# Kernel optimization log

Hardware: AMD Instinct MI355X
Metric: run time of the kernel (lower is better)

The kernel has to match this reference:

```python
import jax, jax.numpy as jnp
import numpy as np

N_NODES = 100000
N_EDGES = 1600000
IN_CH = 61
OUT_CH = 64
BN_EPS = 1e-5


def setup_inputs() -> dict:
    key = jax.random.key(0)
    ks = jax.random.split(key, 8)
    x = jax.random.normal(ks[0], (N_NODES, IN_CH), dtype=jnp.float32)
    pos = jax.random.normal(ks[1], (N_NODES, 3), dtype=jnp.float32)
    edge_index = jax.random.randint(ks[2], (2, N_EDGES), 0, N_NODES, dtype=jnp.int64)
    d_in = 3 + IN_CH  # 64
    W1 = jax.random.normal(ks[3], (d_in, OUT_CH), dtype=jnp.float32) / np.sqrt(d_in)
    b1 = jnp.zeros((OUT_CH,), dtype=jnp.float32)
    g1 = jnp.ones((OUT_CH,), dtype=jnp.float32)
    be1 = jnp.zeros((OUT_CH,), dtype=jnp.float32)
    Wg = jax.random.normal(ks[4], (OUT_CH, 1), dtype=jnp.float32) / np.sqrt(OUT_CH)
    bg = jnp.zeros((1,), dtype=jnp.float32)
    gg = jnp.ones((1,), dtype=jnp.float32)
    bgb = jnp.zeros((1,), dtype=jnp.float32)
    return {"x": x, "pos": pos, "edge_index": edge_index,
            "W1": W1, "b1": b1, "g1": g1, "be1": be1,
            "Wg": Wg, "bg": bg, "gg": gg, "bgb": bgb}


def _bn_act(h, gamma, beta):
    # PyG MLP layer: BatchNorm1d (training-mode batch stats) -> SiLU
    mu = h.mean(axis=0)
    var = h.var(axis=0)
    h = (h - mu) * jax.lax.rsqrt(var + BN_EPS) * gamma + beta
    return jax.nn.silu(h)


def reference(x, pos, edge_index, W1, b1, g1, be1, Wg, bg, gg, bgb):
    src = edge_index[0]  # source node j (messages flow j -> i)
    dst = edge_index[1]  # target node i
    n = x.shape[0]
    # PointNetConv message: local_nn(cat([x_j, pos_j - pos_i]))
    feat = jnp.concatenate([x[src], pos[src] - pos[dst]], axis=-1)  # [E, 3+in]
    h = _bn_act(feat @ W1 + b1, g1, be1)  # [E, out]
    # AttentionalAggregation gate: MLP([out, 1]) per edge
    gate = _bn_act(h @ Wg + bg, gg, bgb)  # [E, 1]
    # segment softmax over destination nodes
    m = jax.ops.segment_max(gate, dst, num_segments=n)  # [N, 1]
    e = jnp.exp(gate - m[dst])
    s = jax.ops.segment_sum(e, dst, num_segments=n)
    alpha = e / (s[dst] + 1e-16)
    # weighted scatter-sum aggregate
    out = jax.ops.segment_sum(alpha * h, dst, num_segments=n)  # [N, out]
    return out
```

## Files before the change

kernel.cpp:

```cpp
#include <hip/hip_runtime.h>
#include <hip/hip_bf16.h>
#include <math.h>

constexpr int N_NODES = 100000;
constexpr int N_EDGES = 1600000;
constexpr int IN_CH   = 61;
constexpr float BN_EPS = 1e-5f;
constexpr int NPART   = 32;

constexpr int S_PH = 192;
constexpr int S_PG = 192 + NPART * 128;
constexpr int S_TOT = S_PG + NPART * 2;

typedef float f32x4 __attribute__((ext_vector_type(4)));
typedef short s16x8 __attribute__((ext_vector_type(8)));

__device__ __forceinline__ float silu(float x) { return x / (1.0f + expf(-x)); }

__device__ __forceinline__ float bf2f(unsigned v) { return __uint_as_float(v << 16); }
__device__ __forceinline__ unsigned f2bf(float f) {
    unsigned u = __float_as_uint(f);
    return (u + 0x7FFFu + ((u >> 16) & 1u)) >> 16;
}

__device__ __forceinline__ bool edge_gemm(
    int e, const float* __restrict__ x, const float* __restrict__ pos,
    const int* __restrict__ ei, const float* __restrict__ W1,
    const float* __restrict__ b1, float* acc, int* jd_out)
{
    int js = ei[e];
    int jd = ei[N_EDGES + e];
    *jd_out = jd;
    bool valid = ((unsigned)js < (unsigned)N_NODES) && ((unsigned)jd < (unsigned)N_NODES);
    if (!valid) {
        #pragma unroll
        for (int c = 0; c < 64; ++c) acc[c] = 0.0f;
        return false;
    }
    #pragma unroll
    for (int c = 0; c < 64; ++c) acc[c] = b1[c];
    const float* xr = x + (size_t)js * IN_CH;
    #pragma unroll 4
    for (int k = 0; k < IN_CH; ++k) {
        float fk = xr[k];
        #pragma unroll
        for (int c = 0; c < 64; ++c) acc[c] += fk * W1[k * 64 + c];
    }
    #pragma unroll
    for (int j = 0; j < 3; ++j) {
        float fk = pos[js * 3 + j] - pos[jd * 3 + j];
        #pragma unroll
        for (int c = 0; c < 64; ++c) acc[c] += fk * W1[(IN_CH + j) * 64 + c];
    }
    return true;
}

__global__ __launch_bounds__(256) void k_init(float* stats, int* deg) {
    int i = blockIdx.x * 256 + threadIdx.x;
    if (i < S_TOT) stats[i] = 0.0f;
    if (i < N_NODES) deg[i] = 0;
}

__global__ __launch_bounds__(256) void k_prep(const float* __restrict__ W1,
                                              short* __restrict__ wf)
{
    int i = blockIdx.x * 256 + threadIdx.x;
    int j    = i & 7;
    int lane = (i >> 3) & 63;
    int kc   = (i >> 9) & 1;
    int ct   = i >> 10;
    int c = ct * 16 + (lane & 15);
    int k = kc * 32 + (lane >> 4) * 8 + j;
    float v = W1[k * 64 + c];
    unsigned hi = f2bf(v);
    unsigned lo = f2bf(v - bf2f(hi));
    wf[i] = (short)hi;
    wf[4096 + i] = (short)lo;
}

__global__ __launch_bounds__(256) void k_edge_mfma(
    const float* __restrict__ x, const float* __restrict__ pos,
    const int* __restrict__ ei, const short* __restrict__ wf,
    const float* __restrict__ b1, float* __restrict__ stats,
    int* __restrict__ deg, void* __restrict__ h, size_t h_cap)
{
    __shared__ __align__(16) short fsh[64][72];
    __shared__ __align__(16) short fsl[64][72];
    __shared__ float lsum[128];

    const int tid  = threadIdx.x;
    const int w    = tid >> 6, lane = tid & 63;
    const int e0   = blockIdx.x * 64;

    if (tid < 128) lsum[tid] = 0.0f;

    int js_l = 0, jd_l = 0;
    if (lane < 16) {
        int e = e0 + w * 16 + lane;
        js_l = ei[e];
        jd_l = ei[N_EDGES + e];
        if ((unsigned)js_l >= (unsigned)N_NODES) js_l = 0;
        if ((unsigned)jd_l >= (unsigned)N_NODES) jd_l = 0;
        atomicAdd(&deg[jd_l], 1);
    }

    #pragma unroll 4
    for (int j = 0; j < 16; ++j) {
        int js = __shfl(js_l, j);
        int jd = __shfl(jd_l, j);
        int r  = w * 16 + j;
        float v;
        if (lane < IN_CH) v = x[(size_t)js * IN_CH + lane];
        else              v = pos[js * 3 + (lane - IN_CH)] - pos[jd * 3 + (lane - IN_CH)];
        unsigned hi = f2bf(v);
        unsigned lo = f2bf(v - bf2f(hi));
        fsh[r][lane] = (short)hi;
        fsl[r][lane] = (short)lo;
    }
    __syncthreads();

    const int r = lane & 15, g = lane >> 4;
    const int arow = w * 16 + r;
    s16x8 ah0 = *(const s16x8*)&fsh[arow][g * 8];
    s16x8 ah1 = *(const s16x8*)&fsh[arow][32 + g * 8];
    s16x8 al0 = *(const s16x8*)&fsl[arow][g * 8];
    s16x8 al1 = *(const s16x8*)&fsl[arow][32 + g * 8];

    const bool do_h = ((size_t)(e0 + 64) * 128 <= h_cap);
    unsigned short* hp = (unsigned short*)h;

    #pragma unroll
    for (int ct = 0; ct < 4; ++ct) {
        int c = ct * 16 + r;
        s16x8 bh0 = *(const s16x8*)&wf[((ct * 2 + 0) * 64 + lane) * 8];
        s16x8 bh1 = *(const s16x8*)&wf[((ct * 2 + 1) * 64 + lane) * 8];
        s16x8 bl0 = *(const s16x8*)&wf[4096 + ((ct * 2 + 0) * 64 + lane) * 8];
        s16x8 bl1 = *(const s16x8*)&wf[4096 + ((ct * 2 + 1) * 64 + lane) * 8];
        f32x4 acc = {0.0f, 0.0f, 0.0f, 0.0f};
        acc = __builtin_amdgcn_mfma_f32_16x16x32_bf16(al0, bh0, acc, 0, 0, 0);
        acc = __builtin_amdgcn_mfma_f32_16x16x32_bf16(al1, bh1, acc, 0, 0, 0);
        acc = __builtin_amdgcn_mfma_f32_16x16x32_bf16(ah0, bl0, acc, 0, 0, 0);
        acc = __builtin_amdgcn_mfma_f32_16x16x32_bf16(ah1, bl1, acc, 0, 0, 0);
        acc = __builtin_amdgcn_mfma_f32_16x16x32_bf16(ah0, bh0, acc, 0, 0, 0);
        acc = __builtin_amdgcn_mfma_f32_16x16x32_bf16(ah1, bh1, acc, 0, 0, 0);
        float bias = b1[c];
        float s = 0.0f, q = 0.0f;
        #pragma unroll
        for (int i = 0; i < 4; ++i) {
            unsigned hb = f2bf(acc[i] + bias);
            float v = bf2f(hb);
            s += v; q += v * v;
            if (do_h) {
                int row = w * 16 + g * 4 + i;
                hp[(size_t)(e0 + row) * 64 + c] = (unsigned short)hb;
            }
        }
        s += __shfl_xor(s, 16); s += __shfl_xor(s, 32);
        q += __shfl_xor(q, 16); q += __shfl_xor(q, 32);
        if (g == 0) {
            atomicAdd(&lsum[c], s);
            atomicAdd(&lsum[64 + c], q);
        }
    }
    __syncthreads();
    if (tid < 128)
        atomicAdd(&stats[S_PH + (blockIdx.x & (NPART - 1)) * 128 + tid], lsum[tid]);
}

template<int MODE>
__global__ __launch_bounds__(128) void k_edge(
    const float* __restrict__ x, const float* __restrict__ pos,
    const int* __restrict__ ei, const float* __restrict__ W1,
    const float* __restrict__ b1, float* __restrict__ stats,
    int* __restrict__ deg, void* __restrict__ h, size_t h_cap)
{
    constexpr int EPB = 128;
    __shared__ float fs[EPB][65];
    __shared__ float ls[128];

    const int tid  = threadIdx.x;
    const int wave = tid >> 6, lane = tid & 63;
    const int eb   = blockIdx.x * EPB;
    const int r0   = wave * 64;

    const int eg = eb + r0 + lane;
    int js_l = ei[eg];
    int jd_l = ei[N_EDGES + eg];
    bool valid = ((unsigned)js_l < (unsigned)N_NODES) &&
                 ((unsigned)jd_l < (unsigned)N_NODES);
    if (valid) atomicAdd(&deg[jd_l], 1);

    if constexpr (MODE == 2) {
        if (tid < 128) ls[tid] = 0.0f;
    }

    for (int j = 0; j < 64; ++j) {
        int js = __shfl(js_l, j);
        int jd = __shfl(jd_l, j);
        int ok = __shfl((int)valid, j);
        int r = r0 + j;
        if (lane < IN_CH) {
            fs[r][lane] = ok ? x[(size_t)js * IN_CH + lane] : 0.0f;
        } else {
            int d = lane - IN_CH;
            fs[r][lane] = ok ? (pos[js * 3 + d] - pos[jd * 3 + d]) : 0.0f;
        }
    }
    __syncthreads();

    #pragma unroll 1
    for (int half = 0; half < 2; ++half) {
        const int base = half * 32;
        float acc[32];
        #pragma unroll
        for (int c = 0; c < 32; ++c) acc[c] = valid ? b1[base + c] : 0.0f;
        if (valid) {
            #pragma unroll 4
            for (int k = 0; k < 64; ++k) {
                float fk = fs[tid][k];
                #pragma unroll
                for (int c = 0; c < 32; ++c)
                    acc[c] += fk * W1[k * 64 + base + c];
            }
        }
        if constexpr (MODE == 0) {
            if ((size_t)(eb + tid + 1) * 256 <= h_cap) {
                float4* hq = (float4*)((char*)h + (size_t)(eb + tid) * 256
                                       + (size_t)base * 4);
                #pragma unroll
                for (int i = 0; i < 8; ++i)
                    hq[i] = make_float4(acc[4*i], acc[4*i+1], acc[4*i+2], acc[4*i+3]);
            }
        } else {
            #pragma unroll
            for (int c = 0; c < 32; ++c) {
                atomicAdd(&ls[base + c], acc[c]);
                atomicAdd(&ls[64 + base + c], acc[c] * acc[c]);
            }
        }
    }

    if constexpr (MODE == 2) {
        __syncthreads();
        if (tid < 128)
            atomicAdd(&stats[S_PH + (blockIdx.x & (NPART-1)) * 128 + tid], ls[tid]);
    }
}

template<int MODE>
__global__ __launch_bounds__(256) void k_stats(const void* __restrict__ h,
                                               float* __restrict__ stats)
{
    constexpr int VEC = (MODE == 0) ? 4 : 8;
    const size_t nvec = (size_t)N_EDGES * 64 / VEC;
    size_t stride = (size_t)gridDim.x * 256;
    size_t g0 = (size_t)blockIdx.x * 256 + threadIdx.x;
    int c0 = (int)((g0 * VEC) & 63);
    float sum[VEC], sq[VEC];
    #pragma unroll
    for (int j = 0; j < VEC; ++j) { sum[j] = 0.0f; sq[j] = 0.0f; }

    for (size_t v = g0; v < nvec; v += stride) {
        float vals[VEC];
        if constexpr (MODE == 0) {
            float4 t = ((const float4*)h)[v];
            vals[0] = t.x; vals[1] = t.y; vals[2] = t.z; vals[3] = t.w;
        } else {
            uint4 t = ((const uint4*)h)[v];
            vals[0] = bf2f(t.x & 0xFFFF); vals[1] = bf2f(t.x >> 16);
            vals[2] = bf2f(t.y & 0xFFFF); vals[3] = bf2f(t.y >> 16);
            vals[4] = bf2f(t.z & 0xFFFF); vals[5] = bf2f(t.z >> 16);
            vals[6] = bf2f(t.w & 0xFFFF); vals[7] = bf2f(t.w >> 16);
        }
        #pragma unroll
        for (int j = 0; j < VEC; ++j) { sum[j] += vals[j]; sq[j] += vals[j] * vals[j]; }
    }
    __shared__ float ls[128];
    if (threadIdx.x < 128) ls[threadIdx.x] = 0.0f;
    __syncthreads();
    #pragma unroll
    for (int j = 0; j < VEC; ++j) {
        atomicAdd(&ls[c0 + j], sum[j]);
        atomicAdd(&ls[64 + c0 + j], sq[j]);
    }
    __syncthreads();
    if (threadIdx.x < 128)
        atomicAdd(&stats[S_PH + (blockIdx.x & (NPART-1)) * 128 + threadIdx.x],
                  ls[threadIdx.x]);
}

__global__ void k_bnfin(float* stats) {
    int c = threadIdx.x;
    if (c < 64) {
        float s = 0.0f, q = 0.0f;
        #pragma unroll
        for (int p = 0; p < NPART; ++p) {
            s += stats[S_PH + p * 128 + c];
            q += stats[S_PH + p * 128 + 64 + c];
        }
        float m = s / (float)N_EDGES;
        float v = q / (float)N_EDGES - m * m;
        stats[c] = m;
        stats[64 + c] = rsqrtf(v + BN_EPS);
    }
}

template<int MODE>
__global__ __launch_bounds__(256) void k_gate(
    const void* __restrict__ h, const float* __restrict__ x,
    const float* __restrict__ pos, const int* __restrict__ ei,
    const float* __restrict__ W1, const float* __restrict__ b1,
    float* __restrict__ stats, const float* __restrict__ g1,
    const float* __restrict__ be1, const float* __restrict__ Wg,
    const float* __restrict__ bg, float* __restrict__ gate_lin, size_t h_cap)
{
    int e = blockIdx.x * 256 + threadIdx.x;
    float gl = bg[0];

    if constexpr (MODE == 2) {
        float hv[64];
        int jd;
        edge_gemm(e, x, pos, ei, W1, b1, hv, &jd);
        #pragma unroll
        for (int c = 0; c < 64; ++c) {
            float t = (hv[c] - stats[c]) * stats[64 + c] * g1[c] + be1[c];
            gl += silu(t) * Wg[c];
        }
    } else if constexpr (MODE == 0) {
        if ((size_t)(e + 1) * 256 <= h_cap) {
            const float4* hq = (const float4*)((const char*)h + (size_t)e * 256);
            #pragma unroll
            for (int i = 0; i < 16; ++i) {
                float4 t = hq[i];
                float vv[4] = {t.x, t.y, t.z, t.w};
                #pragma unroll
                for (int j = 0; j < 4; ++j) {
                    int c = 4 * i + j;
                    float tt = (vv[j] - stats[c]) * stats[64 + c] * g1[c] + be1[c];
                    gl += silu(tt) * Wg[c];
                }
            }
        }
    } else {
        if ((size_t)(e + 1) * 128 <= h_cap) {
            const uint4* hq = (const uint4*)((const char*)h + (size_t)e * 128);
            #pragma unroll
            for (int j = 0; j < 8; ++j) {
                uint4 t = hq[j];
                float vv[8];
                vv[0] = bf2f(t.x & 0xFFFF); vv[1] = bf2f(t.x >> 16);
                vv[2] = bf2f(t.y & 0xFFFF); vv[3] = bf2f(t.y >> 16);
                vv[4] = bf2f(t.z & 0xFFFF); vv[5] = bf2f(t.z >> 16);
                vv[6] = bf2f(t.w & 0xFFFF); vv[7] = bf2f(t.w >> 16);
                #pragma unroll
                for (int q = 0; q < 8; ++q) {
                    int c = 8 * j + q;
                    float tt = (vv[q] - stats[c]) * stats[64 + c] * g1[c] + be1[c];
                    gl += silu(tt) * Wg[c];
                }
            }
        }
    }
    gate_lin[e] = gl;

    float s1 = gl, s2 = gl * gl;
    #pragma unroll
    for (int off = 32; off >= 1; off >>= 1) {
        s1 += __shfl_xor(s1, off);
        s2 += __shfl_xor(s2, off);
    }
    __shared__ float red[8];
    int w = threadIdx.x >> 6, lane = threadIdx.x & 63;
    if (lane == 0) { red[w] = s1; red[4 + w] = s2; }
    __syncthreads();
    if (threadIdx.x == 0) {
        int slot = S_PG + (blockIdx.x & (NPART-1)) * 2;
        atomicAdd(&stats[slot], red[0] + red[1] + red[2] + red[3]);
        atomicAdd(&stats[slot + 1], red[4] + red[5] + red[6] + red[7]);
    }
}

__global__ void k_gfin(float* stats) {
    if (threadIdx.x == 0) {
        float s = 0.0f, q = 0.0f;
        for (int p = 0; p < NPART; ++p) {
            s += stats[S_PG + 2 * p];
            q += stats[S_PG + 2 * p + 1];
        }
        float m = s / (float)N_EDGES;
        float v = q / (float)N_EDGES - m * m;
        stats[128] = m;
        stats[129] = rsqrtf(v + BN_EPS);
    }
}

__global__ __launch_bounds__(1024) void k_scan(const int* __restrict__ deg,
                                               int* __restrict__ offs,
                                               int* __restrict__ cursor)
{
    __shared__ int ps[1024];
    int t = threadIdx.x;
    const int CH = (N_NODES + 1023) / 1024;
    int lo = t * CH, hi = lo + CH;
    if (hi > N_NODES) hi = N_NODES;
    if (lo > N_NODES) lo = N_NODES;
    int s = 0;
    for (int i = lo; i < hi; ++i) s += deg[i];
    ps[t] = s;
    __syncthreads();
    for (int off = 1; off < 1024; off <<= 1) {
        int v = (t >= off) ? ps[t - off] : 0;
        __syncthreads();
        ps[t] += v;
        __syncthreads();
    }
    int run = (t == 0) ? 0 : ps[t - 1];
    for (int i = lo; i < hi; ++i) {
        offs[i] = run;
        cursor[i] = run;
        run += deg[i];
    }
    if (t == 1023) offs[N_NODES] = ps[1023];
}

__global__ __launch_bounds__(256) void k_fill(const int* __restrict__ ei,
                                              int* __restrict__ cursor,
                                              int* __restrict__ elist)
{
    int e = blockIdx.x * 256 + threadIdx.x;
    int js = ei[e];
    int d = ei[N_EDGES + e];
    if ((unsigned)js >= (unsigned)N_NODES || (unsigned)d >= (unsigned)N_NODES) return;
    int p = atomicAdd(&cursor[d], 1);
    if ((unsigned)p < (unsigned)N_EDGES) elist[p] = e;
}

template<int MODE>
__device__ __forceinline__ void aggr_body(
    const void* __restrict__ h, size_t h_cap, const float* __restrict__ gate_lin,
    const int* __restrict__ offs, const int* __restrict__ elist,
    const int* __restrict__ ei, const float* __restrict__ x,
    const float* __restrict__ pos, const float* __restrict__ b1,
    const float* W1s, const float* __restrict__ stats,
    const float* __restrict__ g1, const float* __restrict__ be1,
    const float* __restrict__ gg, const float* __restrict__ bgb,
    float* __restrict__ out)
{
    int wid = (blockIdx.x * 256 + threadIdx.x) >> 6;
    int lane = threadIdx.x & 63;
    if (wid >= N_NODES) return;

    float mu = stats[lane], rs = stats[64 + lane];
    float gmu = stats[128], grs = stats[129];
    float ga = g1[lane], bb = be1[lane];
    float gga = gg[0], gbb = bgb[0];

    int lo = offs[wid], hi = offs[wid + 1];
    float accv = 0.0f, wsum = 0.0f;

    if constexpr (MODE == 2) {
        float b1v = b1[lane];
        float pim = (lane >= IN_CH) ? pos[wid * 3 + (lane - IN_CH)] : 0.0f;
        for (int i = lo; i < hi; ++i) {
            int e = elist[i];
            float gl = gate_lin[e];
            float tg = (gl - gmu) * grs * gga + gbb;
            float w = expf(silu(tg));
            int js = ei[e];
            if ((unsigned)js >= (unsigned)N_NODES) continue;
            float fl = (lane < IN_CH) ? x[(size_t)js * IN_CH + lane]
                                      : pos[js * 3 + (lane - IN_CH)] - pim;
            float a = b1v;
            #pragma unroll
            for (int k = 0; k < 64; ++k) a += __shfl(fl, k) * W1s[k * 64 + lane];
            float tn = (a - mu) * rs * ga + bb;
            accv += w * silu(tn);
            wsum += w;
        }
    } else {
        auto load_h = [&](int e) -> float {
            if constexpr (MODE == 0) {
                if ((size_t)(e + 1) * 256 > h_cap) return 0.0f;
                return ((const float*)h)[(size_t)e * 64 + lane];
            } else {
                if ((size_t)(e + 1) * 128 > h_cap) return 0.0f;
                return bf2f(((const unsigned short*)h)[(size_t)e * 64 + lane]);
            }
        };
        if (lo < hi) {
            int e = elist[lo];
            float gl = gate_lin[e];
            float hval = load_h(e);
            for (int i = lo; i < hi; ++i) {
                int en = 0; float gln = 0.0f, hn = 0.0f;
                if (i + 1 < hi) {
                    en = elist[i + 1];
                    gln = gate_lin[en];
                    hn = load_h(en);
                }
                float tg = (gl - gmu) * grs * gga + gbb;
                float w = expf(silu(tg));
                float tn = (hval - mu) * rs * ga + bb;
                accv += w * silu(tn);
                wsum += w;
                e = en; gl = gln; hval = hn;
            }
        }
    }
    out[(size_t)wid * 64 + lane] = accv / (wsum + 1e-16f);
}

template<int MODE>
__global__ __launch_bounds__(256) void k_aggr(
    const void* __restrict__ h, size_t h_cap, const float* __restrict__ gate_lin,
    const int* __restrict__ offs, const int* __restrict__ elist,
    const int* __restrict__ ei, const float* __restrict__ x,
    const float* __restrict__ pos, const float* __restrict__ b1,
    const float* __restrict__ W1, const float* __restrict__ stats,
    const float* __restrict__ g1, const float* __restrict__ be1,
    const float* __restrict__ gg, const float* __restrict__ bgb,
    float* __restrict__ out)
{
    if constexpr (MODE == 2) {
        __shared__ float W1s[4096];
        for (int i = threadIdx.x; i < 4096; i += 256) W1s[i] = W1[i];
        __syncthreads();
        aggr_body<2>(h, h_cap, gate_lin, offs, elist, ei, x, pos, b1, W1s,
                     stats, g1, be1, gg, bgb, out);
    } else {
        aggr_body<MODE>(h, h_cap, gate_lin, offs, elist, ei, x, pos, b1, nullptr,
                        stats, g1, be1, gg, bgb, out);
    }
}

extern "C" void kernel_launch(void* const* d_in, const int* in_sizes, int n_in,
                              void* d_out, int out_size, void* d_ws, size_t ws_size,
                              hipStream_t stream)
{
    const float* x   = (const float*)d_in[0];
    const float* pos = (const float*)d_in[1];
    const int*   ei  = (const int*)d_in[2];
    const float* W1  = (const float*)d_in[3];
    const float* b1  = (const float*)d_in[4];
    const float* g1  = (const float*)d_in[5];
    const float* be1 = (const float*)d_in[6];
    const float* Wg  = (const float*)d_in[7];
    const float* bg  = (const float*)d_in[8];
    const float* gg  = (const float*)d_in[9];
    const float* bgb = (const float*)d_in[10];
    float* out = (float*)d_out;

    char* base = (char*)d_ws;
    size_t off = 0;
    auto alloc = [&](size_t bytes) {
        size_t o = off;
        off = (off + bytes + 255) & ~(size_t)255;
        return o;
    };
    float* stats    = (float*)(base + alloc(S_TOT * 4));
    int*   deg      = (int*)(base + alloc((size_t)N_NODES * 4));
    int*   offs     = (int*)(base + alloc((size_t)(N_NODES + 1) * 4));
    int*   cursor   = (int*)(base + alloc((size_t)N_NODES * 4));
    int*   elist    = (int*)(base + alloc((size_t)N_EDGES * 4));
    float* gate_lin = (float*)(base + alloc((size_t)N_EDGES * 4));
    short* wfrag    = (short*)(base + alloc(8192 * 2));
    if (ws_size < off) return;
    void*  h     = (void*)(base + off);
    size_t h_cap = ws_size - off;

    const int mode = (h_cap >= (size_t)N_EDGES * 256) ? 0
                   : (h_cap >= (size_t)N_EDGES * 128) ? 1 : 2;

    const int EB  = N_EDGES / 256;
    const int EB2 = N_EDGES / 128;
    const int EBM = N_EDGES / 64;
    const int NB  = (N_NODES + 255) / 256;
    const int AB  = (N_NODES + 3) / 4;

    hipLaunchKernelGGL(k_init, dim3(NB), dim3(256), 0, stream, stats, deg);

    if (mode == 0) {
        hipLaunchKernelGGL(k_edge<0>, dim3(EB2), dim3(128), 0, stream,
                           x, pos, ei, W1, b1, stats, deg, h, h_cap);
        hipLaunchKernelGGL(k_stats<0>, dim3(1024), dim3(256), 0, stream, h, stats);
        hipLaunchKernelGGL(k_bnfin, dim3(1), dim3(64), 0, stream, stats);
        hipLaunchKernelGGL(k_gate<0>, dim3(EB), dim3(256), 0, stream,
                           h, x, pos, ei, W1, b1, stats, g1, be1, Wg, bg, gate_lin, h_cap);
    } else if (mode == 1) {
        hipLaunchKernelGGL(k_prep, dim3(16), dim3(256), 0, stream, W1, wfrag);
        hipLaunchKernelGGL(k_edge_mfma, dim3(EBM), dim3(256), 0, stream,
                           x, pos, ei, wfrag, b1, stats, deg, h, h_cap);
        hipLaunchKernelGGL(k_bnfin, dim3(1), dim3(64), 0, stream, stats);
        hipLaunchKernelGGL(k_gate<1>, dim3(EB), dim3(256), 0, stream,
                           h, x, pos, ei, W1, b1, stats, g1, be1, Wg, bg, gate_lin, h_cap);
    } else {
        hipLaunchKernelGGL(k_edge<2>, dim3(EB2), dim3(128), 0, stream,
                           x, pos, ei, W1, b1, stats, deg, h, h_cap);
        hipLaunchKernelGGL(k_bnfin, dim3(1), dim3(64), 0, stream, stats);
        hipLaunchKernelGGL(k_gate<2>, dim3(EB), dim3(256), 0, stream,
                           h, x, pos, ei, W1, b1, stats, g1, be1, Wg, bg, gate_lin, h_cap);
    }

    hipLaunchKernelGGL(k_gfin, dim3(1), dim3(64), 0, stream, stats);
    hipLaunchKernelGGL(k_scan, dim3(1), dim3(1024), 0, stream, deg, offs, cursor);
    hipLaunchKernelGGL(k_fill, dim3(EB), dim3(256), 0, stream, ei, cursor, elist);

    if (mode == 0) {
        hipLaunchKernelGGL(k_aggr<0>, dim3(AB), dim3(256), 0, stream,
                           h, h_cap, gate_lin, offs, elist, ei, x, pos, b1, W1,
                           stats, g1, be1, gg, bgb, out);
    } else if (mode == 1) {
        hipLaunchKernelGGL(k_aggr<1>, dim3(AB), dim3(256), 0, stream,
                           h, h_cap, gate_lin, offs, elist, ei, x, pos, b1, W1,
                           stats, g1, be1, gg, bgb, out);
    } else {
        hipLaunchKernelGGL(k_aggr<2>, dim3(AB), dim3(256), 0, stream,
                           h, h_cap, gate_lin, offs, elist, ei, x, pos, b1, W1,
                           stats, g1, be1, gg, bgb, out);
    }
}
```

Measured before the change: 1.101 ms.

## Precompute per-edge softmax weights and store activated h in gate pass

The gate kernel now writes the post-BatchNorm SiLU activation back into the h buffer (fp16 instead of bf16 in the compact mode), and a new k_w kernel turns each gate logit into exp(silu(normalized gate)) once per edge. The aggregation kernel then only does a weighted sum of stored activations, with no per-lane BN, SiLU or exp in its gather loop. SiLU also switches to __expf with a hardware reciprocal. This trades an extra write of h and one more small launch for less arithmetic in the latency-bound gather. Fast-math exp, rcp and fp16 storage may shift numerics slightly.

```diff
diff --git a/kernel.cpp b/kernel.cpp
--- a/kernel.cpp
+++ b/kernel.cpp
@@ -1,5 +1,6 @@
 #include <hip/hip_runtime.h>
 #include <hip/hip_bf16.h>
+#include <hip/hip_fp16.h>
 #include <math.h>
 
 constexpr int N_NODES = 100000;
@@ -15,7 +16,10 @@
 typedef float f32x4 __attribute__((ext_vector_type(4)));
 typedef short s16x8 __attribute__((ext_vector_type(8)));
 
-__device__ __forceinline__ float silu(float x) { return x / (1.0f + expf(-x)); }
+__device__ __forceinline__ float fast_exp(float x) { return __expf(x); }
+__device__ __forceinline__ float silu(float x) {
+    return x * __builtin_amdgcn_rcpf(1.0f + __expf(-x));
+}
 
 __device__ __forceinline__ float bf2f(unsigned v) { return __uint_as_float(v << 16); }
 __device__ __forceinline__ unsigned f2bf(float f) {
@@ -307,7 +311,7 @@
 
 template<int MODE>
 __global__ __launch_bounds__(256) void k_gate(
-    const void* __restrict__ h, const float* __restrict__ x,
+    void* __restrict__ h, const float* __restrict__ x,
     const float* __restrict__ pos, const int* __restrict__ ei,
     const float* __restrict__ W1, const float* __restrict__ b1,
     float* __restrict__ stats, const float* __restrict__ g1,
@@ -328,22 +332,25 @@
         }
     } else if constexpr (MODE == 0) {
         if ((size_t)(e + 1) * 256 <= h_cap) {
-            const float4* hq = (const float4*)((const char*)h + (size_t)e * 256);
+            float4* hq = (float4*)((char*)h + (size_t)e * 256);
             #pragma unroll
             for (int i = 0; i < 16; ++i) {
                 float4 t = hq[i];
                 float vv[4] = {t.x, t.y, t.z, t.w};
+                float sv[4];
                 #pragma unroll
                 for (int j = 0; j < 4; ++j) {
                     int c = 4 * i + j;
                     float tt = (vv[j] - stats[c]) * stats[64 + c] * g1[c] + be1[c];
-                    gl += silu(tt) * Wg[c];
+                    sv[j] = silu(tt);
+                    gl += sv[j] * Wg[c];
                 }
+                hq[i] = make_float4(sv[0], sv[1], sv[2], sv[3]);
             }
         }
     } else {
         if ((size_t)(e + 1) * 128 <= h_cap) {
-            const uint4* hq = (const uint4*)((const char*)h + (size_t)e * 128);
+            uint4* hq = (uint4*)((char*)h + (size_t)e * 128);
             #pragma unroll
             for (int j = 0; j < 8; ++j) {
                 uint4 t = hq[j];
@@ -352,12 +359,19 @@
                 vv[2] = bf2f(t.y & 0xFFFF); vv[3] = bf2f(t.y >> 16);
                 vv[4] = bf2f(t.z & 0xFFFF); vv[5] = bf2f(t.z >> 16);
                 vv[6] = bf2f(t.w & 0xFFFF); vv[7] = bf2f(t.w >> 16);
+                unsigned pw[4];
                 #pragma unroll
-                for (int q = 0; q < 8; ++q) {
-                    int c = 8 * j + q;
-                    float tt = (vv[q] - stats[c]) * stats[64 + c] * g1[c] + be1[c];
-                    gl += silu(tt) * Wg[c];
+                for (int q = 0; q < 4; ++q) {
+                    int c0 = 8 * j + 2 * q;
+                    float t0 = (vv[2*q]   - stats[c0])   * stats[64 + c0]   * g1[c0]   + be1[c0];
+                    float t1 = (vv[2*q+1] - stats[c0+1]) * stats[64 + c0+1] * g1[c0+1] + be1[c0+1];
+                    float s0 = silu(t0), s1 = silu(t1);
+                    gl += s0 * Wg[c0] + s1 * Wg[c0 + 1];
+                    unsigned u0 = __half_as_ushort(__float2half(s0));
+                    unsigned u1 = __half_as_ushort(__float2half(s1));
+                    pw[q] = u0 | (u1 << 16);
                 }
+                hq[j] = make_uint4(pw[0], pw[1], pw[2], pw[3]);
             }
         }
     }
@@ -392,6 +406,17 @@
         stats[128] = m;
         stats[129] = rsqrtf(v + BN_EPS);
     }
+}
+
+__global__ __launch_bounds__(256) void k_w(float* __restrict__ gate_lin,
+                                           const float* __restrict__ stats,
+                                           const float* __restrict__ gg,
+                                           const float* __restrict__ bgb)
+{
+    int e = blockIdx.x * 256 + threadIdx.x;
+    float gl = gate_lin[e];
+    float tg = (gl - stats[128]) * stats[129] * gg[0] + bgb[0];
+    gate_lin[e] = fast_exp(silu(tg));
 }
 
 __global__ __launch_bounds__(1024) void k_scan(const int* __restrict__ deg,
@@ -437,35 +462,29 @@
 
 template<int MODE>
 __device__ __forceinline__ void aggr_body(
-    const void* __restrict__ h, size_t h_cap, const float* __restrict__ gate_lin,
+    const void* __restrict__ h, size_t h_cap, const float* __restrict__ wgt,
     const int* __restrict__ offs, const int* __restrict__ elist,
     const int* __restrict__ ei, const float* __restrict__ x,
     const float* __restrict__ pos, const float* __restrict__ b1,
     const float* W1s, const float* __restrict__ stats,
     const float* __restrict__ g1, const float* __restrict__ be1,
-    const float* __restrict__ gg, const float* __restrict__ bgb,
     float* __restrict__ out)
 {
     int wid = (blockIdx.x * 256 + threadIdx.x) >> 6;
     int lane = threadIdx.x & 63;
     if (wid >= N_NODES) return;
 
-    float mu = stats[lane], rs = stats[64 + lane];
-    float gmu = stats[128], grs = stats[129];
-    float ga = g1[lane], bb = be1[lane];
-    float gga = gg[0], gbb = bgb[0];
-
     int lo = offs[wid], hi = offs[wid + 1];
     float accv = 0.0f, wsum = 0.0f;
 
     if constexpr (MODE == 2) {
+        float mu = stats[lane], rs = stats[64 + lane];
+        float ga = g1[lane], bb = be1[lane];
         float b1v = b1[lane];
         float pim = (lane >= IN_CH) ? pos[wid * 3 + (lane - IN_CH)] : 0.0f;
         for (int i = lo; i < hi; ++i) {
             int e = elist[i];
-            float gl = gate_lin[e];
-            float tg = (gl - gmu) * grs * gga + gbb;
-            float w = expf(silu(tg));
+            float w = wgt[e];
             int js = ei[e];
             if ((unsigned)js >= (unsigned)N_NODES) continue;
             float fl = (lane < IN_CH) ? x[(size_t)js * IN_CH + lane]
@@ -484,26 +503,24 @@
                 return ((const float*)h)[(size_t)e * 64 + lane];
             } else {
                 if ((size_t)(e + 1) * 128 > h_cap) return 0.0f;
-                return bf2f(((const unsigned short*)h)[(size_t)e * 64 + lane]);
+                return __half2float(__ushort_as_half(
+                    ((const unsigned short*)h)[(size_t)e * 64 + lane]));
             }
         };
         if (lo < hi) {
             int e = elist[lo];
-            float gl = gate_lin[e];
+            float w = wgt[e];
             float hval = load_h(e);
             for (int i = lo; i < hi; ++i) {
-                int en = 0; float gln = 0.0f, hn = 0.0f;
+                int en = 0; float wn = 0.0f, hn = 0.0f;
                 if (i + 1 < hi) {
                     en = elist[i + 1];
-                    gln = gate_lin[en];
+                    wn = wgt[en];
                     hn = load_h(en);
                 }
-                float tg = (gl - gmu) * grs * gga + gbb;
-                float w = expf(silu(tg));
-                float tn = (hval - mu) * rs * ga + bb;
-                accv += w * silu(tn);
+                accv += w * hval;
                 wsum += w;
-                e = en; gl = gln; hval = hn;
+                e = en; w = wn; hval = hn;
             }
         }
     }
@@ -512,24 +529,23 @@
 
 template<int MODE>
 __global__ __launch_bounds__(256) void k_aggr(
-    const void* __restrict__ h, size_t h_cap, const float* __restrict__ gate_lin,
+    const void* __restrict__ h, size_t h_cap, const float* __restrict__ wgt,
     const int* __restrict__ offs, const int* __restrict__ elist,
     const int* __restrict__ ei, const float* __restrict__ x,
     const float* __restrict__ pos, const float* __restrict__ b1,
     const float* __restrict__ W1, const float* __restrict__ stats,
     const float* __restrict__ g1, const float* __restrict__ be1,
-    const float* __restrict__ gg, const float* __restrict__ bgb,
     float* __restrict__ out)
 {
     if constexpr (MODE == 2) {
         __shared__ float W1s[4096];
         for (int i = threadIdx.x; i < 4096; i += 256) W1s[i] = W1[i];
         __syncthreads();
-        aggr_body<2>(h, h_cap, gate_lin, offs, elist, ei, x, pos, b1, W1s,
-                     stats, g1, be1, gg, bgb, out);
+        aggr_body<2>(h, h_cap, wgt, offs, elist, ei, x, pos, b1, W1s,
+                     stats, g1, be1, out);
     } else {
-        aggr_body<MODE>(h, h_cap, gate_lin, offs, elist, ei, x, pos, b1, nullptr,
-                        stats, g1, be1, gg, bgb, out);
+        aggr_body<MODE>(h, h_cap, wgt, offs, elist, ei, x, pos, b1, nullptr,
+                        stats, g1, be1, out);
     }
 }
 
@@ -602,20 +618,21 @@
     }
 
     hipLaunchKernelGGL(k_gfin, dim3(1), dim3(64), 0, stream, stats);
+    hipLaunchKernelGGL(k_w,    dim3(EB), dim3(256), 0, stream, gate_lin, stats, gg, bgb);
     hipLaunchKernelGGL(k_scan, dim3(1), dim3(1024), 0, stream, deg, offs, cursor);
     hipLaunchKernelGGL(k_fill, dim3(EB), dim3(256), 0, stream, ei, cursor, elist);
 
     if (mode == 0) {
         hipLaunchKernelGGL(k_aggr<0>, dim3(AB), dim3(256), 0, stream,
                            h, h_cap, gate_lin, offs, elist, ei, x, pos, b1, W1,
-                           stats, g1, be1, gg, bgb, out);
+                           stats, g1, be1, out);
     } else if (mode == 1) {
         hipLaunchKernelGGL(k_aggr<1>, dim3(AB), dim3(256), 0, stream,
                            h, h_cap, gate_lin, offs, elist, ei, x, pos, b1, W1,
-                           stats, g1, be1, gg, bgb, out);
+                           stats, g1, be1, out);
     } else {
         hipLaunchKernelGGL(k_aggr<2>, dim3(AB), dim3(256), 0, stream,
                            h, h_cap, gate_lin, offs, elist, ei, x, pos, b1, W1,
-                           stats, g1, be1, gg, bgb, out);
-    }
-}
+                           stats, g1, be1, out);
+    }
+}
```

New measurement: 985.2 us. -10.5%, faster.
